# Kernel optimization log

Measured on AMD Instinct MI355X. Metric: run time of the kernel, lower is better.

The kernel has to match this reference:

```python
import jax, jax.numpy as jnp
import numpy as np

B, NH, WH, WW, C, NPOS = 64, 16, 16, 16, 64, 288
N = WH * WW


def setup_inputs() -> dict:
    key = jax.random.key(0)
    k1, k2, k3 = jax.random.split(key, 3)
    query = jax.random.normal(k1, (B, NH, N, C), dtype=jnp.float32)
    attn_logits = jax.random.normal(k2, (B, NH, N, N), dtype=jnp.float32)
    pos_emb = jax.random.normal(k3, (C, NPOS), dtype=jnp.float32) * 0.02
    return {"query": query, "attn_logits": attn_logits, "pos_emb": pos_emb,
            "Wh": WH, "Ww": WW, "npos_max": NPOS}


def _rev_cumsum(x):
    # flip -> cumsum -> flip along last axis
    return jnp.flip(jnp.cumsum(jnp.flip(x, -1), axis=-1), -1)


def reference(query, attn_logits, pos_emb, Wh, Ww, npos_max):
    B_, nH, N_, C_ = query.shape
    gates = jax.nn.sigmoid(attn_logits)                       # (B,nH,N,N)
    gates_h = gates.swapaxes(-1, -2).reshape(B_, nH, N_, Ww, Wh)
    gates_w = gates.reshape(B_, nH, N_, Wh, Ww)
    pos_h = _rev_cumsum(gates_h).reshape(B_, nH, N_, N_).swapaxes(-1, -2)
    pos_w = _rev_cumsum(gates_w).reshape(B_, nH, N_, N_)
    pos = pos_h * Ww + pos_w
    pos = jnp.minimum(pos, npos_max - 1)
    pos_floor = jnp.floor(pos)
    pos_ceil_i = jnp.ceil(pos).astype(jnp.int32)
    pos_floor_i = pos_floor.astype(jnp.int32)
    # (B,nH,N,C) @ (C,npos) -> (B,nH,N,npos)
    logits_int = jnp.einsum('bhnc,cp->bhnp', query, pos_emb)
    logits_ceil = jnp.take_along_axis(logits_int, pos_ceil_i, axis=-1)
    logits_floor = jnp.take_along_axis(logits_int, pos_floor_i, axis=-1)
    w = pos - pos_floor
    return logits_ceil * w + logits_floor * (1.0 - w)
```

## Files before the change

### kernel.cpp

```cpp
#include <hip/hip_runtime.h>


#define NPOS 288
#define NT   18
#define LTS  288

typedef __attribute__((ext_vector_type(8))) short bf16x8;
typedef __attribute__((ext_vector_type(4))) float f32x4;

__device__ __forceinline__ short f2bf(float f) {
    unsigned u = __float_as_uint(f);
    u += 0x7FFF + ((u >> 16) & 1);
    return (short)(u >> 16);
}

template <int D>
__device__ __forceinline__ float suffix_step(float v) {
    int s = __builtin_amdgcn_update_dpp(0, __float_as_int(v), 0x100 | D, 0xF, 0xF, true);
    return v + __int_as_float(s);
}

__global__ void prep_kernel(const float* __restrict__ pos_emb,
                            short* __restrict__ wsb) {
    int idx = blockIdx.x * blockDim.x + threadIdx.x;
    if (idx >= NT * 2 * 64) return;
    int l = idx & 63;
    int s = (idx >> 6) & 1;
    int t = idx >> 7;
    int col = t * 16 + (l & 15);
    int k0  = s * 32 + (l >> 4) * 8;
    short* dst = wsb + idx * 8;
    #pragma unroll
    for (int j = 0; j < 8; ++j)
        dst[j] = f2bf(pos_emb[(k0 + j) * NPOS + col]);
}

__global__ __launch_bounds__(256, 6) void cope2d_kernel(
    const float* __restrict__ query,
    const float* __restrict__ attn_logits,
    const bf16x8* __restrict__ wsb8,
    float* __restrict__ out)
{
    __shared__ float Ltab[16 * LTS];

    const int tid  = threadIdx.x;
    const int lane = tid & 63;
    const int wave = tid >> 6;
    const int blk  = blockIdx.x;
    const int bh   = blk >> 4;
    const int p    = blk & 15;
    const long rowbase = (long)bh * 256 + p * 16;
    const long gbase   = rowbase * 256;

    const float* qptr = query + (rowbase + (lane & 15)) * 64 + (lane >> 4) * 8;
    bf16x8 A[2];
    #pragma unroll
    for (int s = 0; s < 2; ++s) {
        f32x4 lo = *(const f32x4*)(qptr + s * 32);
        f32x4 hi = *(const f32x4*)(qptr + s * 32 + 4);
        #pragma unroll
        for (int j = 0; j < 4; ++j) { A[s][j] = f2bf(lo[j]); A[s][4 + j] = f2bf(hi[j]); }
    }

    float g[16];
    #pragma unroll
    for (int i = 0; i < 16; ++i)
        g[i] = attn_logits[gbase + (long)i * 256 + tid];

    for (int t = wave; t < NT; t += 4) {
        f32x4 c = {0.f, 0.f, 0.f, 0.f};
        c = __builtin_amdgcn_mfma_f32_16x16x32_bf16(A[0], wsb8[(t * 2 + 0) * 64 + lane], c, 0, 0, 0);
        c = __builtin_amdgcn_mfma_f32_16x16x32_bf16(A[1], wsb8[(t * 2 + 1) * 64 + lane], c, 0, 0, 0);
        const int col = t * 16 + (lane & 15);
        const int r0  = (lane >> 4) * 4;
        #pragma unroll
        for (int r = 0; r < 4; ++r)
            Ltab[(r0 + r) * LTS + col] = c[r];
    }
    __syncthreads();

    {
        #pragma unroll
        for (int i = 0; i < 16; ++i)
            g[i] = 1.0f / (1.0f + __expf(-g[i]));

        float sfx[16];
        float run = 0.f;
        #pragma unroll
        for (int i = 15; i >= 0; --i) { run += g[i]; sfx[i] = run; }

        #pragma unroll
        for (int half = 0; half < 2; ++half) {
            const int i0 = half * 8;
            float w8[8]; int fi8[8];
            #pragma unroll
            for (int k = 0; k < 8; ++k) {
                const int i = i0 + k;
                float pw = suffix_step<8>(suffix_step<4>(suffix_step<2>(suffix_step<1>(g[i]))));
                float pos = fminf(sfx[i] * 16.0f + pw, 287.0f);
                float pf = floorf(pos);
                fi8[k] = (int)pf;
                w8[k]  = pos - pf;
            }
            float lf8[8], lc8[8];
            #pragma unroll
            for (int k = 0; k < 8; ++k) {
                const float* Lr = Ltab + (i0 + k) * LTS;
                lf8[k] = Lr[fi8[k]];
                lc8[k] = Lr[fi8[k] + 1];
            }
            #pragma unroll
            for (int k = 0; k < 8; ++k)
                out[gbase + (long)(i0 + k) * 256 + tid] =
                    lf8[k] + w8[k] * (lc8[k] - lf8[k]);
        }
    }
}

extern "C" void kernel_launch(void* const* d_in, const int* in_sizes, int n_in,
                              void* d_out, int out_size, void* d_ws, size_t ws_size,
                              hipStream_t stream) {
    const float* query       = (const float*)d_in[0];
    const float* attn_logits = (const float*)d_in[1];
    const float* pos_emb     = (const float*)d_in[2];
    float* outp = (float*)d_out;
    short* wsb  = (short*)d_ws;

    prep_kernel<<<9, 256, 0, stream>>>(pos_emb, wsb);
    cope2d_kernel<<<16384, 256, 0, stream>>>(query, attn_logits,
                                             (const bf16x8*)d_ws, outp);
}
```

Baseline: 137.6 us.

## Restructure CoPE kernel to single-wave blocks with bf16 LDS table and streamed gates

```diff
diff --git a/kernel.cpp b/kernel.cpp
--- a/kernel.cpp
+++ b/kernel.cpp
@@ -3,21 +3,41 @@
 
 #define NPOS 288
 #define NT   18
-#define LTS  288
+#define LTS2 292
 
 typedef __attribute__((ext_vector_type(8))) short bf16x8;
 typedef __attribute__((ext_vector_type(4))) float f32x4;
 
-__device__ __forceinline__ short f2bf(float f) {
+__device__ __forceinline__ unsigned short f2bf(float f) {
     unsigned u = __float_as_uint(f);
     u += 0x7FFF + ((u >> 16) & 1);
-    return (short)(u >> 16);
+    return (unsigned short)(u >> 16);
+}
+__device__ __forceinline__ unsigned cvt_pk_bf16(float lo, float hi) {
+    unsigned r;
+    asm("v_cvt_pk_bf16_f32 %0, %1, %2" : "=v"(r) : "v"(lo), "v"(hi));
+    return r;
+}
+__device__ __forceinline__ float fast_exp2(float x) {
+    float r; asm("v_exp_f32 %0, %1" : "=v"(r) : "v"(x)); return r;
+}
+__device__ __forceinline__ float fast_fract(float x) {
+    float r; asm("v_fract_f32 %0, %1" : "=v"(r) : "v"(x)); return r;
+}
+__device__ __forceinline__ float bf2f(unsigned short b) {
+    return __uint_as_float(((unsigned)b) << 16);
+}
+__device__ __forceinline__ float sigmoid_f(float x) {
+    return __builtin_amdgcn_rcpf(1.0f + fast_exp2(x * -1.44269504088896f));
 }
 
 template <int D>
 __device__ __forceinline__ float suffix_step(float v) {
     int s = __builtin_amdgcn_update_dpp(0, __float_as_int(v), 0x100 | D, 0xF, 0xF, true);
     return v + __int_as_float(s);
+}
+__device__ __forceinline__ float suffix16(float v) {
+    return suffix_step<8>(suffix_step<4>(suffix_step<2>(suffix_step<1>(v))));
 }
 
 __global__ void prep_kernel(const float* __restrict__ pos_emb,
@@ -32,88 +52,112 @@
     short* dst = wsb + idx * 8;
     #pragma unroll
     for (int j = 0; j < 8; ++j)
-        dst[j] = f2bf(pos_emb[(k0 + j) * NPOS + col]);
+        dst[j] = (short)f2bf(pos_emb[(k0 + j) * NPOS + col]);
 }
 
-__global__ __launch_bounds__(256, 6) void cope2d_kernel(
+__global__ __launch_bounds__(64, 4) void cope2d_kernel(
     const float* __restrict__ query,
     const float* __restrict__ attn_logits,
     const bf16x8* __restrict__ wsb8,
     float* __restrict__ out)
 {
-    __shared__ float Ltab[16 * LTS];
+    __shared__ unsigned short Lb[16 * LTS2];
 
-    const int tid  = threadIdx.x;
-    const int lane = tid & 63;
-    const int wave = tid >> 6;
-    const int blk  = blockIdx.x;
-    const int bh   = blk >> 4;
-    const int p    = blk & 15;
-    const long rowbase = (long)bh * 256 + p * 16;
-    const long gbase   = rowbase * 256;
+    const int lane  = threadIdx.x;
+    const int blk   = blockIdx.x;
+    const int gbase = blk << 12;
 
-    const float* qptr = query + (rowbase + (lane & 15)) * 64 + (lane >> 4) * 8;
-    bf16x8 A[2];
+    const float* qp = query + (blk << 10) + (lane & 15) * 64 + (lane >> 4) * 8;
+    f32x4 qa = *(const f32x4*)(qp);
+    f32x4 qb = *(const f32x4*)(qp + 4);
+    f32x4 qc = *(const f32x4*)(qp + 32);
+    f32x4 qd = *(const f32x4*)(qp + 36);
+
+    const float* gp0 = attn_logits + gbase + lane;
+    const float* gp1 = gp0 + 4 * 256;
+    const float* gp2 = gp0 + 8 * 256;
+    const float* gp3 = gp0 + 12 * 256;
+
+    float gn[4][4];
     #pragma unroll
-    for (int s = 0; s < 2; ++s) {
-        f32x4 lo = *(const f32x4*)(qptr + s * 32);
-        f32x4 hi = *(const f32x4*)(qptr + s * 32 + 4);
-        #pragma unroll
-        for (int j = 0; j < 4; ++j) { A[s][j] = f2bf(lo[j]); A[s][4 + j] = f2bf(hi[j]); }
+    for (int k = 0; k < 4; ++k) gn[0][k] = gp3[3 * 256 + k * 64];
+    #pragma unroll
+    for (int k = 0; k < 4; ++k) gn[1][k] = gp3[2 * 256 + k * 64];
+    #pragma unroll
+    for (int k = 0; k < 4; ++k) gn[2][k] = gp3[1 * 256 + k * 64];
+    #pragma unroll
+    for (int k = 0; k < 4; ++k) gn[3][k] = gp3[0 * 256 + k * 64];
+
+    union { bf16x8 v; unsigned u[4]; } A0, A1;
+    A0.u[0] = cvt_pk_bf16(qa[0], qa[1]); A0.u[1] = cvt_pk_bf16(qa[2], qa[3]);
+    A0.u[2] = cvt_pk_bf16(qb[0], qb[1]); A0.u[3] = cvt_pk_bf16(qb[2], qb[3]);
+    A1.u[0] = cvt_pk_bf16(qc[0], qc[1]); A1.u[1] = cvt_pk_bf16(qc[2], qc[3]);
+    A1.u[2] = cvt_pk_bf16(qd[0], qd[1]); A1.u[3] = cvt_pk_bf16(qd[2], qd[3]);
+
+    unsigned short* wp = Lb + (lane >> 4) * 4 * LTS2 + (lane & 15);
+    #pragma unroll
+    for (int t = 0; t < NT; ++t) {
+        bf16x8 b0 = wsb8[(t * 2 + 0) * 64 + lane];
+        bf16x8 b1 = wsb8[(t * 2 + 1) * 64 + lane];
+        f32x4 c = {0.f, 0.f, 0.f, 0.f};
+        c = __builtin_amdgcn_mfma_f32_16x16x32_bf16(A0.v, b0, c, 0, 0, 0);
+        c = __builtin_amdgcn_mfma_f32_16x16x32_bf16(A1.v, b1, c, 0, 0, 0);
+        const int off = t * 16;
+        wp[off]            = f2bf(c[0]);
+        wp[off + LTS2]     = f2bf(c[1]);
+        wp[off + 2 * LTS2] = f2bf(c[2]);
+        wp[off + 3 * LTS2] = f2bf(c[3]);
     }
 
-    float g[16];
-    #pragma unroll
-    for (int i = 0; i < 16; ++i)
-        g[i] = attn_logits[gbase + (long)i * 256 + tid];
-
-    for (int t = wave; t < NT; t += 4) {
-        f32x4 c = {0.f, 0.f, 0.f, 0.f};
-        c = __builtin_amdgcn_mfma_f32_16x16x32_bf16(A[0], wsb8[(t * 2 + 0) * 64 + lane], c, 0, 0, 0);
-        c = __builtin_amdgcn_mfma_f32_16x16x32_bf16(A[1], wsb8[(t * 2 + 1) * 64 + lane], c, 0, 0, 0);
-        const int col = t * 16 + (lane & 15);
-        const int r0  = (lane >> 4) * 4;
-        #pragma unroll
-        for (int r = 0; r < 4; ++r)
-            Ltab[(r0 + r) * LTS + col] = c[r];
-    }
     __syncthreads();
 
-    {
-        #pragma unroll
-        for (int i = 0; i < 16; ++i)
-            g[i] = 1.0f / (1.0f + __expf(-g[i]));
+    float* op0 = out + gbase + lane;
+    float* op1 = op0 + 4 * 256;
+    float* op2 = op0 + 8 * 256;
+    float* op3 = op0 + 12 * 256;
 
-        float sfx[16];
-        float run = 0.f;
-        #pragma unroll
-        for (int i = 15; i >= 0; --i) { run += g[i]; sfx[i] = run; }
+    float acc0 = 0.f, acc1 = 0.f, acc2 = 0.f, acc3 = 0.f;
+    #pragma unroll
+    for (int r = 15; r >= 0; --r) {
+        const int slot = (15 - r) & 3;
+        float g0 = sigmoid_f(gn[slot][0]);
+        float g1 = sigmoid_f(gn[slot][1]);
+        float g2 = sigmoid_f(gn[slot][2]);
+        float g3 = sigmoid_f(gn[slot][3]);
 
-        #pragma unroll
-        for (int half = 0; half < 2; ++half) {
-            const int i0 = half * 8;
-            float w8[8]; int fi8[8];
+        if (r >= 4) {
+            const int rr = r - 4;
+            const float* gpb = (rr >= 8) ? gp2 : (rr >= 4) ? gp1 : gp0;
             #pragma unroll
-            for (int k = 0; k < 8; ++k) {
-                const int i = i0 + k;
-                float pw = suffix_step<8>(suffix_step<4>(suffix_step<2>(suffix_step<1>(g[i]))));
-                float pos = fminf(sfx[i] * 16.0f + pw, 287.0f);
-                float pf = floorf(pos);
-                fi8[k] = (int)pf;
-                w8[k]  = pos - pf;
-            }
-            float lf8[8], lc8[8];
-            #pragma unroll
-            for (int k = 0; k < 8; ++k) {
-                const float* Lr = Ltab + (i0 + k) * LTS;
-                lf8[k] = Lr[fi8[k]];
-                lc8[k] = Lr[fi8[k] + 1];
-            }
-            #pragma unroll
-            for (int k = 0; k < 8; ++k)
-                out[gbase + (long)(i0 + k) * 256 + tid] =
-                    lf8[k] + w8[k] * (lc8[k] - lf8[k]);
+            for (int k = 0; k < 4; ++k)
+                gn[slot][k] = gpb[(rr & 3) * 256 + k * 64];
         }
+
+        acc0 += g0; acc1 += g1; acc2 += g2; acc3 += g3;
+
+        float pw0 = suffix16(g0), pw1 = suffix16(g1);
+        float pw2 = suffix16(g2), pw3 = suffix16(g3);
+
+        float pos0 = acc0 * 16.0f + pw0;
+        float pos1 = acc1 * 16.0f + pw1;
+        float pos2 = acc2 * 16.0f + pw2;
+        float pos3 = acc3 * 16.0f + pw3;
+        int fi0 = (int)pos0, fi1 = (int)pos1, fi2 = (int)pos2, fi3 = (int)pos3;
+        float w0 = fast_fract(pos0), w1 = fast_fract(pos1);
+        float w2 = fast_fract(pos2), w3 = fast_fract(pos3);
+
+        const unsigned short* Lr = Lb + r * LTS2;
+        float lf0 = bf2f(Lr[fi0]), lc0 = bf2f(Lr[fi0 + 1]);
+        float lf1 = bf2f(Lr[fi1]), lc1 = bf2f(Lr[fi1 + 1]);
+        float lf2 = bf2f(Lr[fi2]), lc2 = bf2f(Lr[fi2 + 1]);
+        float lf3 = bf2f(Lr[fi3]), lc3 = bf2f(Lr[fi3 + 1]);
+
+        float* opb = (r >= 12) ? op3 : (r >= 8) ? op2 : (r >= 4) ? op1 : op0;
+        const int ro = (r & 3) * 256;
+        opb[ro]       = lf0 + w0 * (lc0 - lf0);
+        opb[ro + 64]  = lf1 + w1 * (lc1 - lf1);
+        opb[ro + 128] = lf2 + w2 * (lc2 - lf2);
+        opb[ro + 192] = lf3 + w3 * (lc3 - lf3);
     }
 }
 
@@ -127,6 +171,6 @@
     short* wsb  = (short*)d_ws;
 
     prep_kernel<<<9, 256, 0, stream>>>(pos_emb, wsb);
-    cope2d_kernel<<<16384, 256, 0, stream>>>(query, attn_logits,
-                                             (const bf16x8*)d_ws, outp);
+    cope2d_kernel<<<16384, 64, 0, stream>>>(query, attn_logits,
+                                            (const bf16x8*)d_ws, outp);
 }
```

After: 131.4 us. -4.5%, faster.
